# Performance work log

Measured on AMD Instinct MI355X. Metric: run time of the kernel, lower is better.

The kernel has to match this reference:

```python
import jax, jax.numpy as jnp
import numpy as np

L, B, D_DEC, D_ALIGN, D_ENC = 2048, 64, 1024, 512, 1024


def setup_inputs() -> dict:
    key = jax.random.key(0)
    ks = jax.random.split(key, 8)
    s_tm1 = jax.random.normal(ks[0], (B, D_DEC), dtype=jnp.float32)
    xs_h = jax.random.normal(ks[1], (L, B, D_ENC), dtype=jnp.float32)
    uh = jax.random.normal(ks[2], (L, B, D_ALIGN), dtype=jnp.float32)
    # binary padding mask over source positions; guarantee >=1 valid position per column
    xs_mask = (jax.random.uniform(ks[3], (L, B)) > 0.1).astype(jnp.float32)
    xs_mask = xs_mask.at[0].set(1.0)
    sa_w = jax.random.normal(ks[4], (D_ALIGN, D_DEC), dtype=jnp.float32) / np.sqrt(D_DEC)
    sa_b = jnp.zeros((D_ALIGN,), dtype=jnp.float32)
    a1_w = jax.random.normal(ks[5], (1, D_ALIGN), dtype=jnp.float32) / np.sqrt(D_ALIGN)
    a1_b = jnp.zeros((1,), dtype=jnp.float32)
    return {"s_tm1": s_tm1, "xs_h": xs_h, "uh": uh, "xs_mask": xs_mask,
            "sa_w": sa_w, "sa_b": sa_b, "a1_w": a1_w, "a1_b": a1_b}


def reference(s_tm1, xs_h, uh, xs_mask, sa_w, sa_b, a1_w, a1_b):
    # sa(s_tm1): (B, A)
    proj = s_tm1 @ sa_w.T + sa_b
    # broadcast add over source positions, tanh: (L, B, A)
    act = jnp.tanh(proj[None, :, :] + uh)
    # a1(...).squeeze(2): (L, B)
    score = jnp.einsum('lba,a->lb', act, a1_w[0]) + a1_b[0]
    # masked softmax over dim 0 (exp * mask, then normalize) as in MaskSoftmax
    e = jnp.exp(score - jnp.max(score, axis=0, keepdims=True)) * xs_mask
    e_ij = e / jnp.sum(e, axis=0, keepdims=True)
    # weighted sum of encoder states: (B, D_ENC)
    attend = jnp.einsum('lb,lbd->bd', e_ij, xs_h)
    return (e_ij, attend)
```

## Files before the change

### kernel.cpp

```cpp
#include <hip/hip_runtime.h>

#define L 2048
#define B 64
#define D_DEC 1024
#define D_ALIGN 512
#define D_ENC 1024

using u32 = unsigned int;
using u16 = unsigned short;

__device__ __forceinline__ u16 f2bf(float f) {
    u32 u = __float_as_uint(f);
    u32 r = (u + 0x7fffu + ((u >> 16) & 1u)) >> 16;
    return (u16)r;
}
__device__ __forceinline__ float tanh_fast(float x) {
    float t = __expf(2.0f * x);
    return 1.0f - 2.0f * __builtin_amdgcn_rcpf(t + 1.0f);
}
__device__ __forceinline__ bool detect_bf(const void* xs_mask) {
    return ((const u32*)xs_mask)[0] == 0x3F803F80u;
}
__device__ __forceinline__ float ldv(const void* p, size_t i, bool bf) {
    if (bf) return __uint_as_float(((u32)((const u16*)p)[i]) << 16);
    return ((const float*)p)[i];
}

__global__ __launch_bounds__(256) void proj_kernel(const void* __restrict__ s_tm1,
                                                   const void* __restrict__ sa_w,
                                                   const void* __restrict__ c0,
                                                   const void* __restrict__ c1,
                                                   const void* __restrict__ xs_mask,
                                                   float* __restrict__ proj) {
    bool bf = detect_bf(xs_mask);
    u32 w0 = ((const u32*)c0)[0], w1 = ((const u32*)c1)[0];
    const void* sab = (w0 == 0u || w1 != 0u) ? c0 : c1;
    int idx = blockIdx.x * 256 + threadIdx.x;
    int b = idx >> 9, a = idx & 511;
    size_t sbase = (size_t)b * D_DEC, wbase = (size_t)a * D_DEC;
    float acc = 0.f;
#pragma unroll 8
    for (int k = 0; k < D_DEC; ++k)
        acc += ldv(s_tm1, sbase + k, bf) * ldv(sa_w, wbase + k, bf);
    proj[idx] = acc + ldv(sab, a, bf);
}

__global__ __launch_bounds__(256) void score_kernel(const void* __restrict__ uh,
                                                    const void* __restrict__ c0,
                                                    const void* __restrict__ c1,
                                                    const void* __restrict__ a1_b,
                                                    const void* __restrict__ xs_mask,
                                                    const float* __restrict__ proj,
                                                    float* __restrict__ score) {
    bool bf = detect_bf(xs_mask);
    u32 w0 = ((const u32*)c0)[0], w1 = ((const u32*)c1)[0];
    const void* a1w = (w1 != 0u || w0 == 0u) ? c1 : c0;
    int wave = blockIdx.x * 4 + (threadIdx.x >> 6);
    int lane = threadIdx.x & 63;
    int b = wave & (B - 1);
    int lc = wave >> 6;
    float p[8], w[8];
#pragma unroll
    for (int j = 0; j < 8; ++j) {
        p[j] = proj[b * D_ALIGN + j * 64 + lane];
        w[j] = ldv(a1w, j * 64 + lane, bf);
    }
    float bias = ldv(a1_b, 0, bf);
    float s[8];
#pragma unroll
    for (int il = 0; il < 8; ++il) {
        int l = lc * 8 + il;
        size_t base = (size_t)(l * B + b) * D_ALIGN;
        float v = 0.f;
#pragma unroll
        for (int j = 0; j < 8; ++j)
            v += tanh_fast(p[j] + ldv(uh, base + j * 64 + lane, bf)) * w[j];
        s[il] = v;
    }
#pragma unroll
    for (int il = 0; il < 8; ++il) {
        float v = s[il];
        for (int off = 32; off; off >>= 1) v += __shfl_xor(v, off, 64);
        s[il] = v;
    }
    if (lane == 0) {
#pragma unroll
        for (int il = 0; il < 8; ++il)
            score[(lc * 8 + il) * B + b] = s[il] + bias;
    }
}

__global__ __launch_bounds__(256) void softmax_kernel(const void* __restrict__ xs_mask,
                                                      const float* __restrict__ score,
                                                      float* __restrict__ e_norm,
                                                      void* __restrict__ out) {
    bool bf = detect_bf(xs_mask);
    int b = blockIdx.x;
    int tid = threadIdx.x;
    __shared__ float red[256];
    float s[8];
    float mx = -1e30f;
#pragma unroll
    for (int i = 0; i < 8; ++i) {
        int l = tid + i * 256;
        s[i] = score[l * B + b];
        mx = fmaxf(mx, s[i]);
    }
    red[tid] = mx; __syncthreads();
    for (int off = 128; off; off >>= 1) {
        if (tid < off) red[tid] = fmaxf(red[tid], red[tid + off]);
        __syncthreads();
    }
    mx = red[0]; __syncthreads();
    float sum = 0.f;
#pragma unroll
    for (int i = 0; i < 8; ++i) {
        int l = tid + i * 256;
        s[i] = __expf(s[i] - mx) * ldv(xs_mask, (size_t)l * B + b, bf);
        sum += s[i];
    }
    red[tid] = sum; __syncthreads();
    for (int off = 128; off; off >>= 1) {
        if (tid < off) red[tid] += red[tid + off];
        __syncthreads();
    }
    float inv = 1.0f / red[0];
#pragma unroll
    for (int i = 0; i < 8; ++i) {
        int l = tid + i * 256;
        float e = s[i] * inv;
        e_norm[l * B + b] = e;
        if (bf) ((u16*)out)[l * B + b] = f2bf(e);
        else    ((float*)out)[l * B + b] = e;
    }
}

__global__ __launch_bounds__(256) void attend_kernel(const void* __restrict__ xs_h,
                                                     const void* __restrict__ xs_mask,
                                                     const float* __restrict__ e_norm,
                                                     float* __restrict__ acc) {
    bool bf = detect_bf(xs_mask);
    int b = blockIdx.x & (B - 1);
    int ls = blockIdx.x >> 6;
    int tid = threadIdx.x;
    float a[4] = {0.f, 0.f, 0.f, 0.f};
    int lbeg = ls * (L / 16), lend = lbeg + (L / 16);
    for (int l = lbeg; l < lend; ++l) {
        float w = e_norm[l * B + b];
        size_t base = (size_t)(l * B + b) * D_ENC;
#pragma unroll
        for (int j = 0; j < 4; ++j)
            a[j] += w * ldv(xs_h, base + tid + j * 256, bf);
    }
#pragma unroll
    for (int j = 0; j < 4; ++j)
        atomicAdd(acc + b * D_ENC + tid + j * 256, a[j]);
}

__global__ __launch_bounds__(256) void finalize_kernel(const float* __restrict__ acc,
                                                       const void* __restrict__ xs_mask,
                                                       void* __restrict__ out) {
    bool bf = detect_bf(xs_mask);
    int i = blockIdx.x * 256 + threadIdx.x;
    if (bf) ((u16*)out)[(size_t)L * B + i] = f2bf(acc[i]);
    else    ((float*)out)[(size_t)L * B + i] = acc[i];
}

extern "C" void kernel_launch(void* const* d_in, const int* in_sizes, int n_in,
                              void* d_out, int out_size, void* d_ws, size_t ws_size,
                              hipStream_t stream) {
    const void *s_tm1 = d_in[0], *xs_h = d_in[1], *uh = d_in[2], *xs_mask = d_in[3],
               *sa_w = d_in[4];
    const void *a1_b = d_in[7];
    const void *p512[2] = {d_in[5], d_in[6]};
    int n512 = 0;
    for (int i = 0; i < n_in; ++i) {
        switch (in_sizes[i]) {
            case 134217728: xs_h = d_in[i]; break;
            case 67108864:  uh = d_in[i]; break;
            case 131072:    xs_mask = d_in[i]; break;
            case 65536:     s_tm1 = d_in[i]; break;
            case 524288:    sa_w = d_in[i]; break;
            case 1:         a1_b = d_in[i]; break;
            case 512:       if (n512 < 2) p512[n512] = d_in[i]; ++n512; break;
            default: break;
        }
    }
    const void* c0 = p512[0];
    const void* c1 = p512[1];

    char* ws = (char*)d_ws;
    float* proj   = (float*)(ws);
    float* score  = (float*)(ws + 131072);
    float* e_norm = (float*)(ws + 131072 + 524288);
    float* acc    = (float*)(ws + 131072 + 1048576);

    hipMemsetAsync(acc, 0, D_ENC * B * sizeof(float), stream);

    proj_kernel<<<128, 256, 0, stream>>>(s_tm1, sa_w, c0, c1, xs_mask, proj);
    score_kernel<<<4096, 256, 0, stream>>>(uh, c0, c1, a1_b, xs_mask, proj, score);
    softmax_kernel<<<B, 256, 0, stream>>>(xs_mask, score, e_norm, d_out);
    attend_kernel<<<1024, 256, 0, stream>>>(xs_h, xs_mask, e_norm, acc);
    finalize_kernel<<<256, 256, 0, stream>>>(acc, xs_mask, d_out);
}
```

Measured before the change: 970.3 us.

## Vectorize loads, restructure projection GEMV, replace atomics with partial-sum reduction

The projection kernel becomes a wave-per-row GEMV with float4 loads and shuffle reductions instead of one strided thread per output. The score and attend kernels use float4 loads of uh and xs_h in the fp32 path. Scores and softmax weights are stored transposed (b-major) so each batch column reads contiguously. The attend stage writes per-split partials, combined by a separate reduce kernel, which removes the atomics, the memset and the finalize kernel. The cost is extra workspace and one more pass over the partial buffer.

Result: faster. 873.2 us (-10.0%).

```diff
diff --git a/kernel.cpp b/kernel.cpp
--- a/kernel.cpp
+++ b/kernel.cpp
@@ -5,6 +5,7 @@
 #define D_DEC 1024
 #define D_ALIGN 512
 #define D_ENC 1024
+#define LSPLIT 32
 
 using u32 = unsigned int;
 using u16 = unsigned short;
@@ -35,14 +36,43 @@
     bool bf = detect_bf(xs_mask);
     u32 w0 = ((const u32*)c0)[0], w1 = ((const u32*)c1)[0];
     const void* sab = (w0 == 0u || w1 != 0u) ? c0 : c1;
-    int idx = blockIdx.x * 256 + threadIdx.x;
-    int b = idx >> 9, a = idx & 511;
-    size_t sbase = (size_t)b * D_DEC, wbase = (size_t)a * D_DEC;
-    float acc = 0.f;
-#pragma unroll 8
-    for (int k = 0; k < D_DEC; ++k)
-        acc += ldv(s_tm1, sbase + k, bf) * ldv(sa_w, wbase + k, bf);
-    proj[idx] = acc + ldv(sab, a, bf);
+    int b = blockIdx.x >> 3;
+    int wid = threadIdx.x >> 6, lane = threadIdx.x & 63;
+    int a0 = (blockIdx.x & 7) * 64 + wid * 16;
+    size_t sb = (size_t)b * D_DEC + (size_t)lane * 16;
+    float sreg[16];
+    if (!bf) {
+        const float4* s4 = (const float4*)((const float*)s_tm1 + sb);
+#pragma unroll
+        for (int m = 0; m < 4; ++m) {
+            float4 v = s4[m];
+            sreg[4*m] = v.x; sreg[4*m+1] = v.y; sreg[4*m+2] = v.z; sreg[4*m+3] = v.w;
+        }
+    } else {
+#pragma unroll
+        for (int m = 0; m < 16; ++m) sreg[m] = ldv(s_tm1, sb + m, bf);
+    }
+#pragma unroll 4
+    for (int ai = 0; ai < 16; ++ai) {
+        int a = a0 + ai;
+        size_t wb = (size_t)a * D_DEC + (size_t)lane * 16;
+        float acc = 0.f;
+        if (!bf) {
+            const float4* w4 = (const float4*)((const float*)sa_w + wb);
+#pragma unroll
+            for (int m = 0; m < 4; ++m) {
+                float4 v = w4[m];
+                acc += sreg[4*m] * v.x + sreg[4*m+1] * v.y
+                     + sreg[4*m+2] * v.z + sreg[4*m+3] * v.w;
+            }
+        } else {
+#pragma unroll
+            for (int m = 0; m < 16; ++m) acc += sreg[m] * ldv(sa_w, wb + m, bf);
+        }
+#pragma unroll
+        for (int off = 32; off; off >>= 1) acc += __shfl_xor(acc, off, 64);
+        if (lane == 0) proj[b * D_ALIGN + a] = acc + ldv(sab, a, bf);
+    }
 }
 
 __global__ __launch_bounds__(256) void score_kernel(const void* __restrict__ uh,
@@ -51,7 +81,7 @@
                                                     const void* __restrict__ a1_b,
                                                     const void* __restrict__ xs_mask,
                                                     const float* __restrict__ proj,
-                                                    float* __restrict__ score) {
+                                                    float* __restrict__ score_t) {
     bool bf = detect_bf(xs_mask);
     u32 w0 = ((const u32*)c0)[0], w1 = ((const u32*)c1)[0];
     const void* a1w = (w1 != 0u || w0 == 0u) ? c1 : c0;
@@ -59,40 +89,64 @@
     int lane = threadIdx.x & 63;
     int b = wave & (B - 1);
     int lc = wave >> 6;
-    float p[8], w[8];
-#pragma unroll
-    for (int j = 0; j < 8; ++j) {
-        p[j] = proj[b * D_ALIGN + j * 64 + lane];
-        w[j] = ldv(a1w, j * 64 + lane, bf);
-    }
     float bias = ldv(a1_b, 0, bf);
     float s[8];
-#pragma unroll
-    for (int il = 0; il < 8; ++il) {
-        int l = lc * 8 + il;
-        size_t base = (size_t)(l * B + b) * D_ALIGN;
-        float v = 0.f;
-#pragma unroll
-        for (int j = 0; j < 8; ++j)
-            v += tanh_fast(p[j] + ldv(uh, base + j * 64 + lane, bf)) * w[j];
-        s[il] = v;
+    if (!bf) {
+        const float4* p4 = (const float4*)proj + (size_t)b * 128;
+        const float4* w4 = (const float4*)a1w;
+        float4 p[2], w[2];
+#pragma unroll
+        for (int j = 0; j < 2; ++j) { p[j] = p4[j * 64 + lane]; w[j] = w4[j * 64 + lane]; }
+#pragma unroll
+        for (int il = 0; il < 8; ++il) {
+            int l = lc * 8 + il;
+            const float4* u4 = (const float4*)uh + (size_t)(l * B + b) * 128;
+            float v = 0.f;
+#pragma unroll
+            for (int j = 0; j < 2; ++j) {
+                float4 u = u4[j * 64 + lane];
+                v += tanh_fast(p[j].x + u.x) * w[j].x;
+                v += tanh_fast(p[j].y + u.y) * w[j].y;
+                v += tanh_fast(p[j].z + u.z) * w[j].z;
+                v += tanh_fast(p[j].w + u.w) * w[j].w;
+            }
+            s[il] = v;
+        }
+    } else {
+        float p[8], w[8];
+#pragma unroll
+        for (int j = 0; j < 8; ++j) {
+            p[j] = proj[b * D_ALIGN + j * 64 + lane];
+            w[j] = ldv(a1w, j * 64 + lane, bf);
+        }
+#pragma unroll
+        for (int il = 0; il < 8; ++il) {
+            int l = lc * 8 + il;
+            size_t base = (size_t)(l * B + b) * D_ALIGN;
+            float v = 0.f;
+#pragma unroll
+            for (int j = 0; j < 8; ++j)
+                v += tanh_fast(p[j] + ldv(uh, base + j * 64 + lane, bf)) * w[j];
+            s[il] = v;
+        }
     }
 #pragma unroll
     for (int il = 0; il < 8; ++il) {
         float v = s[il];
+#pragma unroll
         for (int off = 32; off; off >>= 1) v += __shfl_xor(v, off, 64);
         s[il] = v;
     }
     if (lane == 0) {
 #pragma unroll
         for (int il = 0; il < 8; ++il)
-            score[(lc * 8 + il) * B + b] = s[il] + bias;
+            score_t[(size_t)b * L + lc * 8 + il] = s[il] + bias;
     }
 }
 
 __global__ __launch_bounds__(256) void softmax_kernel(const void* __restrict__ xs_mask,
-                                                      const float* __restrict__ score,
-                                                      float* __restrict__ e_norm,
+                                                      const float* __restrict__ score_t,
+                                                      float* __restrict__ e_t,
                                                       void* __restrict__ out) {
     bool bf = detect_bf(xs_mask);
     int b = blockIdx.x;
@@ -102,8 +156,7 @@
     float mx = -1e30f;
 #pragma unroll
     for (int i = 0; i < 8; ++i) {
-        int l = tid + i * 256;
-        s[i] = score[l * B + b];
+        s[i] = score_t[(size_t)b * L + tid + i * 256];
         mx = fmaxf(mx, s[i]);
     }
     red[tid] = mx; __syncthreads();
@@ -129,41 +182,64 @@
     for (int i = 0; i < 8; ++i) {
         int l = tid + i * 256;
         float e = s[i] * inv;
-        e_norm[l * B + b] = e;
-        if (bf) ((u16*)out)[l * B + b] = f2bf(e);
-        else    ((float*)out)[l * B + b] = e;
+        e_t[(size_t)b * L + l] = e;
+        if (bf) ((u16*)out)[(size_t)l * B + b] = f2bf(e);
+        else    ((float*)out)[(size_t)l * B + b] = e;
     }
 }
 
 __global__ __launch_bounds__(256) void attend_kernel(const void* __restrict__ xs_h,
                                                      const void* __restrict__ xs_mask,
-                                                     const float* __restrict__ e_norm,
-                                                     float* __restrict__ acc) {
+                                                     const float* __restrict__ e_t,
+                                                     float* __restrict__ partial) {
     bool bf = detect_bf(xs_mask);
     int b = blockIdx.x & (B - 1);
     int ls = blockIdx.x >> 6;
     int tid = threadIdx.x;
-    float a[4] = {0.f, 0.f, 0.f, 0.f};
-    int lbeg = ls * (L / 16), lend = lbeg + (L / 16);
-    for (int l = lbeg; l < lend; ++l) {
-        float w = e_norm[l * B + b];
-        size_t base = (size_t)(l * B + b) * D_ENC;
-#pragma unroll
-        for (int j = 0; j < 4; ++j)
-            a[j] += w * ldv(xs_h, base + tid + j * 256, bf);
-    }
-#pragma unroll
-    for (int j = 0; j < 4; ++j)
-        atomicAdd(acc + b * D_ENC + tid + j * 256, a[j]);
-}
-
-__global__ __launch_bounds__(256) void finalize_kernel(const float* __restrict__ acc,
-                                                       const void* __restrict__ xs_mask,
-                                                       void* __restrict__ out) {
-    bool bf = detect_bf(xs_mask);
-    int i = blockIdx.x * 256 + threadIdx.x;
-    if (bf) ((u16*)out)[(size_t)L * B + i] = f2bf(acc[i]);
-    else    ((float*)out)[(size_t)L * B + i] = acc[i];
+    float ax = 0.f, ay = 0.f, az = 0.f, aw = 0.f;
+    int lbeg = ls * (L / LSPLIT), lend = lbeg + (L / LSPLIT);
+    if (!bf) {
+        const float4* x4 = (const float4*)xs_h;
+#pragma unroll 4
+        for (int l = lbeg; l < lend; ++l) {
+            float wgt = e_t[(size_t)b * L + l];
+            float4 x = x4[(size_t)(l * B + b) * 256 + tid];
+            ax += wgt * x.x; ay += wgt * x.y; az += wgt * x.z; aw += wgt * x.w;
+        }
+    } else {
+#pragma unroll 2
+        for (int l = lbeg; l < lend; ++l) {
+            float wgt = e_t[(size_t)b * L + l];
+            size_t base = (size_t)(l * B + b) * D_ENC + (size_t)tid * 4;
+            ax += wgt * ldv(xs_h, base + 0, bf);
+            ay += wgt * ldv(xs_h, base + 1, bf);
+            az += wgt * ldv(xs_h, base + 2, bf);
+            aw += wgt * ldv(xs_h, base + 3, bf);
+        }
+    }
+    float4 r; r.x = ax; r.y = ay; r.z = az; r.w = aw;
+    ((float4*)partial)[(size_t)(ls * B + b) * 256 + tid] = r;
+}
+
+__global__ __launch_bounds__(256) void reduce_kernel(const float* __restrict__ partial,
+                                                     const void* __restrict__ xs_mask,
+                                                     void* __restrict__ out) {
+    bool bf = detect_bf(xs_mask);
+    int idx = blockIdx.x * 256 + threadIdx.x;
+    const float4* p4 = (const float4*)partial;
+    float ax = 0.f, ay = 0.f, az = 0.f, aw = 0.f;
+#pragma unroll
+    for (int ls = 0; ls < LSPLIT; ++ls) {
+        float4 v = p4[(size_t)ls * (B * D_ENC / 4) + idx];
+        ax += v.x; ay += v.y; az += v.z; aw += v.w;
+    }
+    if (bf) {
+        u16* o = (u16*)out + (size_t)L * B + (size_t)idx * 4;
+        o[0] = f2bf(ax); o[1] = f2bf(ay); o[2] = f2bf(az); o[3] = f2bf(aw);
+    } else {
+        float4 r; r.x = ax; r.y = ay; r.z = az; r.w = aw;
+        ((float4*)((float*)out + (size_t)L * B))[idx] = r;
+    }
 }
 
 extern "C" void kernel_launch(void* const* d_in, const int* in_sizes, int n_in,
@@ -189,17 +265,14 @@
     const void* c0 = p512[0];
     const void* c1 = p512[1];
 
-    char* ws = (char*)d_ws;
-    float* proj   = (float*)(ws);
-    float* score  = (float*)(ws + 131072);
-    float* e_norm = (float*)(ws + 131072 + 524288);
-    float* acc    = (float*)(ws + 131072 + 1048576);
-
-    hipMemsetAsync(acc, 0, D_ENC * B * sizeof(float), stream);
-
-    proj_kernel<<<128, 256, 0, stream>>>(s_tm1, sa_w, c0, c1, xs_mask, proj);
-    score_kernel<<<4096, 256, 0, stream>>>(uh, c0, c1, a1_b, xs_mask, proj, score);
-    softmax_kernel<<<B, 256, 0, stream>>>(xs_mask, score, e_norm, d_out);
-    attend_kernel<<<1024, 256, 0, stream>>>(xs_h, xs_mask, e_norm, acc);
-    finalize_kernel<<<256, 256, 0, stream>>>(acc, xs_mask, d_out);
-}
+    float* proj    = (float*)d_ws;
+    float* score_t = proj + 32768;
+    float* e_t     = score_t + (size_t)L * B;
+    float* partial = e_t + (size_t)L * B;
+
+    proj_kernel<<<512, 256, 0, stream>>>(s_tm1, sa_w, c0, c1, xs_mask, proj);
+    score_kernel<<<4096, 256, 0, stream>>>(uh, c0, c1, a1_b, xs_mask, proj, score_t);
+    softmax_kernel<<<B, 256, 0, stream>>>(xs_mask, score_t, e_t, d_out);
+    attend_kernel<<<LSPLIT * B, 256, 0, stream>>>(xs_h, xs_mask, e_t, partial);
+    reduce_kernel<<<64, 256, 0, stream>>>(partial, xs_mask, d_out);
+}
```
